# Kernel optimization log

Hardware: AMD Instinct MI355X
Metric: run time of the kernel (lower is better)

Reference implementation:

```python
import jax, jax.numpy as jnp
import numpy as np
import math

IN_CH = 256
CH = 128
SCALE = math.sqrt(CH)
TEMPERATURE = 1.0


def setup_inputs() -> dict:
    key = jax.random.key(0)
    ks = jax.random.split(key, 9)
    B, C, H, W = 8, IN_CH, 56, 56
    x = jax.random.normal(ks[0], (B, C, H, W), dtype=jnp.float32)
    s_in = 1.0 / math.sqrt(IN_CH)
    s_ch = 1.0 / math.sqrt(CH)
    wq = jax.random.uniform(ks[1], (CH, IN_CH), minval=-s_in, maxval=s_in)
    bq = jax.random.uniform(ks[2], (CH,), minval=-s_in, maxval=s_in)
    wk = jax.random.uniform(ks[3], (CH, IN_CH), minval=-s_in, maxval=s_in)
    bk = jax.random.uniform(ks[4], (CH,), minval=-s_in, maxval=s_in)
    wv = jax.random.uniform(ks[5], (CH, IN_CH), minval=-s_in, maxval=s_in)
    bv = jax.random.uniform(ks[6], (CH,), minval=-s_in, maxval=s_in)
    wo = jax.random.uniform(ks[7], (IN_CH, CH), minval=-s_ch, maxval=s_ch)
    bo = jax.random.uniform(ks[8], (IN_CH,), minval=-s_ch, maxval=s_ch)
    return {"x": x, "wq": wq, "bq": bq, "wk": wk, "bk": bk,
            "wv": wv, "bv": bv, "wo": wo, "bo": bo}


def reference(x, wq, bq, wk, bk, wv, bv, wo, bo):
    B, C, H, W = x.shape
    N = H * W
    xf = x.reshape(B, C, N)  # flatten spatial; 1x1 conv == channel matmul
    q = jnp.einsum('oc,bcn->bon', wq, xf) + bq[None, :, None]  # (B,CH,N)
    k = jnp.einsum('oc,bcn->bon', wk, xf) + bk[None, :, None]
    v = jnp.einsum('oc,bcn->bon', wv, xf) + bv[None, :, None]
    # similarity map (B, N, N): query positions x key positions
    sim = jnp.einsum('bcn,bcm->bnm', q, k) / (SCALE * TEMPERATURE)
    attn = jax.nn.softmax(sim, axis=2)
    out = jnp.einsum('bnm,bcm->bnc', attn, v)  # (B, N, CH)
    out = jnp.einsum('oc,bnc->bon', wo, out) + bo[None, :, None]  # (B,IN_CH,N)
    return x + out.reshape(B, C, H, W)
```

## Files before the change

kernel.cpp:

```cpp
#include <hip/hip_runtime.h>
#include <hip/hip_bf16.h>
#include <math.h>

#define NPOS 3136
#define NB   8
#define LOG2E 1.44269504088896f
#define QSCALE (0.08838834764831845f * LOG2E)
#define OFS2  11.54156032711168f

typedef __attribute__((ext_vector_type(8))) short shortx8;
typedef __attribute__((ext_vector_type(4))) short shortx4;
typedef __attribute__((ext_vector_type(4))) float f32x4;
typedef __attribute__((ext_vector_type(16))) float f32x16;
typedef __attribute__((ext_vector_type(4))) unsigned int uint4v;

struct S8pair { shortx4 lo, hi; };

__device__ __forceinline__ unsigned short f2bf(float f) {
    unsigned int i = __builtin_bit_cast(unsigned int, f);
    i += 0x7FFFu + ((i >> 16) & 1u);
    return (unsigned short)(i >> 16);
}
__device__ __forceinline__ void gll16(const unsigned short* g, unsigned short* l) {
    __builtin_amdgcn_global_load_lds((const __attribute__((address_space(1))) void*)g,
                                     (__attribute__((address_space(3))) void*)l, 16, 0, 0);
}

__global__ __launch_bounds__(256) void cast_w(
    const float* __restrict__ wq, const float* __restrict__ wk,
    const float* __restrict__ wv, const float* __restrict__ wo,
    unsigned short* __restrict__ Wb)
{
    const int sel = blockIdx.y;
    const float* src = (sel == 0) ? wq : (sel == 1) ? wk : (sel == 2) ? wv : wo;
    const float sc = (sel == 0) ? QSCALE : 1.0f;
    unsigned short* dst = Wb + sel * 32768;
    int i0 = (blockIdx.x * 256 + threadIdx.x) * 8;
    #pragma unroll
    for (int e = 0; e < 8; ++e) dst[i0 + e] = f2bf(src[i0 + e] * sc);
}

__global__ __launch_bounds__(256) void cast_xT(
    const float* __restrict__ x, unsigned short* __restrict__ xT)
{
    const int b = blockIdx.z, c0 = blockIdx.y * 64, n0 = blockIdx.x * 64;
    __shared__ unsigned short Ls[64 * 66];
    const int t = threadIdx.x;
    {
        int r = t >> 2, q4 = t & 3;
        const float* src = x + ((size_t)b * 256 + c0 + r) * NPOS + n0 + q4 * 16;
        #pragma unroll
        for (int i = 0; i < 16; ++i) Ls[r * 66 + q4 * 16 + i] = f2bf(src[i]);
    }
    __syncthreads();
    {
        int j = t >> 2, h4 = t & 3;
        shortx8 v0, v1;
        #pragma unroll
        for (int i = 0; i < 8; ++i) v0[i] = (short)Ls[(h4 * 16 + i) * 66 + j];
        #pragma unroll
        for (int i = 0; i < 8; ++i) v1[i] = (short)Ls[(h4 * 16 + 8 + i) * 66 + j];
        unsigned short* dst = xT + ((size_t)b * NPOS + n0 + j) * 256 + c0 + h4 * 16;
        *reinterpret_cast<shortx8*>(dst) = v0;
        *reinterpret_cast<shortx8*>(dst + 8) = v1;
    }
}

__global__ __launch_bounds__(256) void qkv_mfma(
    const unsigned short* __restrict__ xT,
    const unsigned short* __restrict__ Wb,
    const float* __restrict__ bq, const float* __restrict__ bk, const float* __restrict__ bv,
    unsigned short* __restrict__ qT, unsigned short* __restrict__ kT,
    unsigned short* __restrict__ vC)
{
    const int b = blockIdx.z, sel = blockIdx.y, n0 = blockIdx.x * 64;
    const int t = threadIdx.x, lane = t & 63, wave = t >> 6;
    const int l16 = lane & 15, lhi = lane >> 4;
    __shared__ __align__(16) unsigned short Wt[128 * 128];
    __shared__ __align__(16) unsigned short Xt[64 * 128];
    const unsigned short* Wsel = Wb + sel * 32768;
    const float* bias = (sel == 0) ? bq : (sel == 1) ? bk : bv;

    f32x4 acc[2][4];
    #pragma unroll
    for (int ab = 0; ab < 2; ++ab)
        #pragma unroll
        for (int nb = 0; nb < 4; ++nb) acc[ab][nb] = f32x4{0.f, 0.f, 0.f, 0.f};

    for (int ks0 = 0; ks0 < 2; ++ks0) {
        const int k0 = ks0 * 128;
        __syncthreads();
        #pragma unroll
        for (int i = 0; i < 8; ++i) {
            int c = (wave * 8 + i) * 64 + lane;
            int row = c >> 4, cin = (c & 15) ^ (row & 7);
            gll16(Wsel + (size_t)row * 256 + k0 + cin * 8, &Wt[0] + (wave * 8 + i) * 512);
        }
        #pragma unroll
        for (int i = 0; i < 4; ++i) {
            int c = (wave * 4 + i) * 64 + lane;
            int row = c >> 4, cin = (c & 15) ^ (row & 7);
            gll16(xT + ((size_t)b * NPOS + n0 + row) * 256 + k0 + cin * 8,
                  &Xt[0] + (wave * 4 + i) * 512);
        }
        __syncthreads();
        #pragma unroll
        for (int ks = 0; ks < 4; ++ks) {
            shortx8 aW[2];
            #pragma unroll
            for (int ab = 0; ab < 2; ++ab) {
                int row = wave * 32 + ab * 16 + l16;
                int idx = (row * 128 + ks * 32 + lhi * 8) ^ ((row & 7) << 3);
                aW[ab] = *reinterpret_cast<const shortx8*>(Wt + idx);
            }
            #pragma unroll
            for (int nb = 0; nb < 4; ++nb) {
                int row = nb * 16 + l16;
                int idx = (row * 128 + ks * 32 + lhi * 8) ^ ((row & 7) << 3);
                shortx8 bX = *reinterpret_cast<const shortx8*>(Xt + idx);
                acc[0][nb] = __builtin_amdgcn_mfma_f32_16x16x32_bf16(aW[0], bX, acc[0][nb], 0, 0, 0);
                acc[1][nb] = __builtin_amdgcn_mfma_f32_16x16x32_bf16(aW[1], bX, acc[1][nb], 0, 0, 0);
            }
        }
    }
    const int strip = wave * 32;
    if (sel < 2) {
        unsigned short* dst0 = ((sel == 0) ? qT : kT) + (size_t)b * NPOS * 128;
        const float bsc = (sel == 0) ? QSCALE : 1.0f;
        #pragma unroll
        for (int ab = 0; ab < 2; ++ab) {
            int ocb = strip + ab * 16 + lhi * 4;
            float bb[4];
            #pragma unroll
            for (int j = 0; j < 4; ++j) bb[j] = bias[ocb + j] * bsc;
            #pragma unroll
            for (int nb = 0; nb < 4; ++nb) {
                int n = n0 + nb * 16 + l16;
                shortx4 u;
                #pragma unroll
                for (int j = 0; j < 4; ++j) u[j] = (short)f2bf(acc[ab][nb][j] + bb[j]);
                *reinterpret_cast<shortx4*>(dst0 + (size_t)n * 128 + ocb) = u;
            }
        }
    } else {
        #pragma unroll
        for (int ab = 0; ab < 2; ++ab)
            #pragma unroll
            for (int j = 0; j < 4; ++j) {
                int oc = strip + ab * 16 + lhi * 4 + j;
                float bb = bias[oc];
                unsigned short* dst = vC + ((size_t)b * 128 + oc) * NPOS + n0;
                #pragma unroll
                for (int nb = 0; nb < 4; ++nb)
                    dst[nb * 16 + l16] = f2bf(acc[ab][nb][j] + bb);
            }
    }
}

__global__ __launch_bounds__(256) void attn_kernel(
    const unsigned short* __restrict__ qT,
    const unsigned short* __restrict__ kT,
    const unsigned short* __restrict__ vC,
    unsigned short* __restrict__ ao,
    float* __restrict__ lrG)
{
    const int b = blockIdx.y, n0 = blockIdx.x * 64;
    const int t = threadIdx.x, lane = t & 63, wave = t >> 6;
    const int l31 = lane & 31, h = lane >> 5;
    const int qsub = wave >> 1, kh = wave & 1;

    __shared__ __align__(16) unsigned short KsB[2][64 * 128];
    __shared__ __align__(16) unsigned short VsB[2][128 * 64];

    shortx8 aQ[8];
    {
        const unsigned short* qp = qT + ((size_t)b * NPOS + n0 + qsub * 32 + l31) * 128 + h * 8;
        #pragma unroll
        for (int kk = 0; kk < 8; ++kk)
            aQ[kk] = *reinterpret_cast<const shortx8*>(qp + kk * 16);
    }

    const unsigned short* kSrc[4];
    const unsigned short* vSrc[4];
    unsigned sDst[4];
    #pragma unroll
    for (int i = 0; i < 4; ++i) {
        int c = (wave * 4 + i) * 64 + lane;
        int rK = c >> 4, cK = (c & 15) ^ (rK & 15);
        kSrc[i] = kT + ((size_t)b * NPOS + rK) * 128 + cK * 8;
        int rV = c >> 3, cV = (c & 7) ^ (rV & 7);
        vSrc[i] = vC + ((size_t)b * 128 + rV) * NPOS + cV * 8;
        sDst[i] = (wave * 4 + i) * 512;
    }

    unsigned kIdx[8];
    {
        int rowK = kh * 32 + l31;
        #pragma unroll
        for (int kk = 0; kk < 8; ++kk)
            kIdx[kk] = rowK * 128 + (((kk * 2 + h) ^ (rowK & 15)) * 8);
    }
    unsigned vIdx[4][2][2];
    #pragma unroll
    for (int ob = 0; ob < 4; ++ob) {
        int rowV = ob * 32 + l31;
        #pragma unroll
        for (int ks = 0; ks < 2; ++ks)
            #pragma unroll
            for (int rr = 0; rr < 2; ++rr)
                vIdx[ob][ks][rr] = rowV * 64 + (((kh * 4 + ks * 2 + rr) ^ (rowV & 7)) * 8) + h * 4;
    }

    f32x16 o[4];
    #pragma unroll
    for (int ob = 0; ob < 4; ++ob)
        #pragma unroll
        for (int r = 0; r < 16; ++r) o[ob][r] = 0.f;
    float lrP = 0.f;

    #pragma unroll
    for (int i = 0; i < 4; ++i) {
        gll16(kSrc[i], &KsB[0][0] + sDst[i]);
        gll16(vSrc[i], &VsB[0][0] + sDst[i]);
    }
    __syncthreads();

    int cur = 0;
    for (int kt = 0; kt < NPOS / 64; ++kt) {
        if (kt + 1 < NPOS / 64) {
            const int m1 = (kt + 1) * 64;
            #pragma unroll
            for (int i = 0; i < 4; ++i) {
                gll16(kSrc[i] + (size_t)m1 * 128, &KsB[cur ^ 1][0] + sDst[i]);
                gll16(vSrc[i] + m1, &VsB[cur ^ 1][0] + sDst[i]);
            }
        }
        const unsigned short* Ks = &KsB[cur][0];
        const unsigned short* Vs = &VsB[cur][0];

        f32x16 sA, sB;
        #pragma unroll
        for (int r = 0; r < 16; ++r) { sA[r] = 0.f; sB[r] = 0.f; }
        #pragma unroll
        for (int kk = 0; kk < 8; kk += 2) {
            shortx8 k0 = *reinterpret_cast<const shortx8*>(Ks + kIdx[kk]);
            shortx8 k1 = *reinterpret_cast<const shortx8*>(Ks + kIdx[kk + 1]);
            sA = __builtin_amdgcn_mfma_f32_32x32x16_bf16(k0, aQ[kk], sA, 0, 0, 0);
            sB = __builtin_amdgcn_mfma_f32_32x32x16_bf16(k1, aQ[kk + 1], sB, 0, 0, 0);
        }

        unsigned pk[8];
        #pragma unroll
        for (int g = 0; g < 4; ++g) {
            float p0 = exp2f(sA[g * 4 + 0] + sB[g * 4 + 0] - OFS2);
            float p1 = exp2f(sA[g * 4 + 1] + sB[g * 4 + 1] - OFS2);
            float p2 = exp2f(sA[g * 4 + 2] + sB[g * 4 + 2] - OFS2);
            float p3 = exp2f(sA[g * 4 + 3] + sB[g * 4 + 3] - OFS2);
            lrP += (p0 + p1) + (p2 + p3);
            asm("v_cvt_pk_bf16_f32 %0, %1, %2" : "=v"(pk[g * 2 + 0]) : "v"(p0), "v"(p1));
            asm("v_cvt_pk_bf16_f32 %0, %1, %2" : "=v"(pk[g * 2 + 1]) : "v"(p2), "v"(p3));
        }

        #pragma unroll
        for (int ks = 0; ks < 2; ++ks) {
            uint4v pv = {pk[ks * 4 + 0], pk[ks * 4 + 1], pk[ks * 4 + 2], pk[ks * 4 + 3]};
            shortx8 PA = __builtin_bit_cast(shortx8, pv);
            #pragma unroll
            for (int ob = 0; ob < 4; ++ob) {
                shortx4 lo = *reinterpret_cast<const shortx4*>(Vs + vIdx[ob][ks][0]);
                shortx4 hi = *reinterpret_cast<const shortx4*>(Vs + vIdx[ob][ks][1]);
                shortx8 bV = __builtin_bit_cast(shortx8, S8pair{lo, hi});
                o[ob] = __builtin_amdgcn_mfma_f32_32x32x16_bf16(PA, bV, o[ob], 0, 0, 0);
            }
        }
        __syncthreads();
        cur ^= 1;
    }

    float lr2 = lrP + __shfl_xor(lrP, 32);
    float* Om = reinterpret_cast<float*>(&KsB[0][0]);
    float* lrS = reinterpret_cast<float*>(&VsB[1][0]);
    unsigned short* Oo = &VsB[0][0];

    if (kh == 1) {
        #pragma unroll
        for (int ob = 0; ob < 4; ++ob)
            #pragma unroll
            for (int r = 0; r < 16; ++r) {
                int q = qsub * 32 + (r & 3) + 8 * (r >> 2) + 4 * h;
                Om[q * 128 + ob * 32 + l31] = o[ob][r];
            }
        if (lane < 32) lrS[qsub * 32 + l31] = lr2;
    }
    __syncthreads();
    if (kh == 0) {
        #pragma unroll
        for (int ob = 0; ob < 4; ++ob)
            #pragma unroll
            for (int r = 0; r < 16; ++r) {
                int q = qsub * 32 + (r & 3) + 8 * (r >> 2) + 4 * h;
                int idx = q * 128 + ob * 32 + l31;
                Oo[idx] = f2bf(o[ob][r] + Om[idx]);
            }
        if (lane < 32)
            lrG[(size_t)b * NPOS + n0 + qsub * 32 + l31] = lr2 + lrS[qsub * 32 + l31];
    }
    __syncthreads();
    {
        const shortx8* src = reinterpret_cast<const shortx8*>(Oo);
        shortx8* dst = reinterpret_cast<shortx8*>(ao + ((size_t)b * NPOS + n0) * 128);
        #pragma unroll
        for (int i = 0; i < 4; ++i) dst[t + 256 * i] = src[t + 256 * i];
    }
}

__global__ __launch_bounds__(256) void out_proj(
    const float* __restrict__ x,
    const unsigned short* __restrict__ Wb,
    const float* __restrict__ bo,
    const unsigned short* __restrict__ ao,
    const float* __restrict__ lrG,
    float* __restrict__ y)
{
    const int b = blockIdx.y, n0 = blockIdx.x * 64;
    const int t = threadIdx.x, lane = t & 63, wave = t >> 6;
    const int l16 = lane & 15, lhi = lane >> 4;
    __shared__ __align__(16) unsigned short Wt[256 * 128];
    __shared__ __align__(16) unsigned short At[64 * 128];
    const unsigned short* wo = Wb + 98304;

    #pragma unroll
    for (int i = 0; i < 16; ++i) {
        int c = (wave * 16 + i) * 64 + lane;
        int row = c >> 4, cin = (c & 15) ^ (row & 7);
        gll16(wo + (size_t)row * 128 + cin * 8, &Wt[0] + (wave * 16 + i) * 512);
    }
    #pragma unroll
    for (int i = 0; i < 4; ++i) {
        int c = (wave * 4 + i) * 64 + lane;
        int row = c >> 4, cin = (c & 15) ^ (row & 7);
        gll16(ao + ((size_t)b * NPOS + n0 + row) * 128 + cin * 8, &At[0] + (wave * 4 + i) * 512);
    }
    __syncthreads();

    f32x4 acc[4][4];
    #pragma unroll
    for (int ab = 0; ab < 4; ++ab)
        #pragma unroll
        for (int nb = 0; nb < 4; ++nb) acc[ab][nb] = f32x4{0.f, 0.f, 0.f, 0.f};

    const int strip = wave * 64;
    #pragma unroll
    for (int ks = 0; ks < 4; ++ks) {
        shortx8 aW[4];
        #pragma unroll
        for (int ab = 0; ab < 4; ++ab) {
            int row = strip + ab * 16 + l16;
            int idx = (row * 128 + ks * 32 + lhi * 8) ^ ((row & 7) << 3);
            aW[ab] = *reinterpret_cast<const shortx8*>(Wt + idx);
        }
        #pragma unroll
        for (int nb = 0; nb < 4; ++nb) {
            int row = nb * 16 + l16;
            int idx = (row * 128 + ks * 32 + lhi * 8) ^ ((row & 7) << 3);
            shortx8 bA = *reinterpret_cast<const shortx8*>(At + idx);
            #pragma unroll
            for (int ab = 0; ab < 4; ++ab)
                acc[ab][nb] = __builtin_amdgcn_mfma_f32_16x16x32_bf16(aW[ab], bA, acc[ab][nb], 0, 0, 0);
        }
    }

    float inv[4];
    #pragma unroll
    for (int nb = 0; nb < 4; ++nb)
        inv[nb] = 1.0f / lrG[(size_t)b * NPOS + n0 + nb * 16 + l16];

    #pragma unroll
    for (int ab = 0; ab < 4; ++ab)
        #pragma unroll
        for (int j = 0; j < 4; ++j) {
            int oc = strip + ab * 16 + lhi * 4 + j;
            float bb = bo[oc];
            const float* xr = x + ((size_t)b * 256 + oc) * NPOS + n0;
            float* yr = y + ((size_t)b * 256 + oc) * NPOS + n0;
            #pragma unroll
            for (int nb = 0; nb < 4; ++nb) {
                int n = nb * 16 + l16;
                yr[n] = xr[n] + bb + acc[ab][nb][j] * inv[nb];
            }
        }
}

extern "C" void kernel_launch(void* const* d_in, const int* in_sizes, int n_in,
                              void* d_out, int out_size, void* d_ws, size_t ws_size,
                              hipStream_t stream)
{
    const float* x  = (const float*)d_in[0];
    const float* wq = (const float*)d_in[1];
    const float* bq = (const float*)d_in[2];
    const float* wk = (const float*)d_in[3];
    const float* bk = (const float*)d_in[4];
    const float* wv = (const float*)d_in[5];
    const float* bv = (const float*)d_in[6];
    const float* wo = (const float*)d_in[7];
    const float* bo = (const float*)d_in[8];
    float* y = (float*)d_out;

    const size_t sz = (size_t)NB * NPOS * 128;
    unsigned short* qT = (unsigned short*)d_ws;
    unsigned short* kT = qT + sz;
    unsigned short* vC = kT + sz;
    unsigned short* xT = vC + sz;
    unsigned short* ao = xT;
    unsigned short* Wb = xT + 2 * sz;
    float* lrG = (float*)(Wb + 131072);

    cast_w  <<<dim3(16, 4),       256, 0, stream>>>(wq, wk, wv, wo, Wb);
    cast_xT <<<dim3(49, 4, NB),   256, 0, stream>>>(x, xT);
    qkv_mfma<<<dim3(49, 3, NB),   256, 0, stream>>>(xT, Wb, bq, bk, bv, qT, kT, vC);
    attn_kernel<<<dim3(49, NB),   256, 0, stream>>>(qT, kT, vC, ao, lrG);
    out_proj<<<dim3(49, NB),      256, 0, stream>>>(x, Wb, bo, ao, lrG, y);
}
```

Measured before the change: 130.1 us.

## Split attention key range across two blocks and merge partial outputs

Launches the attention kernel with a second grid dimension that splits the 49 key tiles into two halves, doubling the block count from 392 to 784 so more of the GPU's compute units get work. Each half writes its own bf16 partial output and row-sum, and a new merge kernel adds the two outputs before out_proj sums the row-sums. To fit more blocks per CU, LDS is cut to a single buffer (no double-buffered prefetch) and launch bounds request 4 blocks per CU. In exchange it loses load/compute overlap, adds an extra kernel pass over the output, and adds bf16 rounding of the partial sums.

```diff
diff --git a/kernel.cpp b/kernel.cpp
--- a/kernel.cpp
+++ b/kernel.cpp
@@ -16,6 +16,10 @@
 
 struct S8pair { shortx4 lo, hi; };
 
+__device__ __forceinline__ float bf2f(unsigned short u) {
+    unsigned int i = ((unsigned int)u) << 16;
+    return __builtin_bit_cast(float, i);
+}
 __device__ __forceinline__ unsigned short f2bf(float f) {
     unsigned int i = __builtin_bit_cast(unsigned int, f);
     i += 0x7FFFu + ((i >> 16) & 1u);
@@ -157,20 +161,23 @@
     }
 }
 
-__global__ __launch_bounds__(256) void attn_kernel(
+__global__ __launch_bounds__(256, 4) void attn_kernel(
     const unsigned short* __restrict__ qT,
     const unsigned short* __restrict__ kT,
     const unsigned short* __restrict__ vC,
     unsigned short* __restrict__ ao,
     float* __restrict__ lrG)
 {
-    const int b = blockIdx.y, n0 = blockIdx.x * 64;
+    const int b = blockIdx.y, n0 = blockIdx.x * 64, z = blockIdx.z;
+    const int kt0 = z ? 25 : 0, kt1 = z ? 49 : 25;
     const int t = threadIdx.x, lane = t & 63, wave = t >> 6;
     const int l31 = lane & 31, h = lane >> 5;
     const int qsub = wave >> 1, kh = wave & 1;
 
-    __shared__ __align__(16) unsigned short KsB[2][64 * 128];
-    __shared__ __align__(16) unsigned short VsB[2][128 * 64];
+    __shared__ __align__(16) unsigned short SM[64 * 128 * 2 + 128];
+    unsigned short* Ks = SM;
+    unsigned short* Vs = SM + 8192;
+    float* lrS = reinterpret_cast<float*>(SM + 16384);
 
     shortx8 aQ[8];
     {
@@ -180,16 +187,14 @@
             aQ[kk] = *reinterpret_cast<const shortx8*>(qp + kk * 16);
     }
 
-    const unsigned short* kSrc[4];
-    const unsigned short* vSrc[4];
-    unsigned sDst[4];
+    unsigned kOff[4], vOff[4], sDst[4];
     #pragma unroll
     for (int i = 0; i < 4; ++i) {
         int c = (wave * 4 + i) * 64 + lane;
         int rK = c >> 4, cK = (c & 15) ^ (rK & 15);
-        kSrc[i] = kT + ((size_t)b * NPOS + rK) * 128 + cK * 8;
+        kOff[i] = ((unsigned)b * NPOS + rK) * 128 + cK * 8;
         int rV = c >> 3, cV = (c & 7) ^ (rV & 7);
-        vSrc[i] = vC + ((size_t)b * 128 + rV) * NPOS + cV * 8;
+        vOff[i] = ((unsigned)b * 128 + rV) * NPOS + cV * 8;
         sDst[i] = (wave * 4 + i) * 512;
     }
 
@@ -200,15 +205,12 @@
         for (int kk = 0; kk < 8; ++kk)
             kIdx[kk] = rowK * 128 + (((kk * 2 + h) ^ (rowK & 15)) * 8);
     }
-    unsigned vIdx[4][2][2];
+    unsigned vBase[4], vM8[4];
     #pragma unroll
     for (int ob = 0; ob < 4; ++ob) {
         int rowV = ob * 32 + l31;
-        #pragma unroll
-        for (int ks = 0; ks < 2; ++ks)
-            #pragma unroll
-            for (int rr = 0; rr < 2; ++rr)
-                vIdx[ob][ks][rr] = rowV * 64 + (((kh * 4 + ks * 2 + rr) ^ (rowV & 7)) * 8) + h * 4;
+        vBase[ob] = rowV * 64 + h * 4;
+        vM8[ob] = (rowV & 7) * 8;
     }
 
     f32x16 o[4];
@@ -218,25 +220,18 @@
         for (int r = 0; r < 16; ++r) o[ob][r] = 0.f;
     float lrP = 0.f;
 
-    #pragma unroll
-    for (int i = 0; i < 4; ++i) {
-        gll16(kSrc[i], &KsB[0][0] + sDst[i]);
-        gll16(vSrc[i], &VsB[0][0] + sDst[i]);
-    }
-    __syncthreads();
-
-    int cur = 0;
-    for (int kt = 0; kt < NPOS / 64; ++kt) {
-        if (kt + 1 < NPOS / 64) {
-            const int m1 = (kt + 1) * 64;
+    for (int kt = kt0; kt < kt1; ++kt) {
+        if (kt > kt0) __syncthreads();
+        {
+            const unsigned short* kP = kT + (size_t)kt * 8192;
+            const unsigned short* vP = vC + kt * 64;
             #pragma unroll
             for (int i = 0; i < 4; ++i) {
-                gll16(kSrc[i] + (size_t)m1 * 128, &KsB[cur ^ 1][0] + sDst[i]);
-                gll16(vSrc[i] + m1, &VsB[cur ^ 1][0] + sDst[i]);
-            }
-        }
-        const unsigned short* Ks = &KsB[cur][0];
-        const unsigned short* Vs = &VsB[cur][0];
+                gll16(kP + kOff[i], Ks + sDst[i]);
+                gll16(vP + vOff[i], Vs + sDst[i]);
+            }
+        }
+        __syncthreads();
 
         f32x16 sA, sB;
         #pragma unroll
@@ -267,28 +262,26 @@
             shortx8 PA = __builtin_bit_cast(shortx8, pv);
             #pragma unroll
             for (int ob = 0; ob < 4; ++ob) {
-                shortx4 lo = *reinterpret_cast<const shortx4*>(Vs + vIdx[ob][ks][0]);
-                shortx4 hi = *reinterpret_cast<const shortx4*>(Vs + vIdx[ob][ks][1]);
+                unsigned i0 = vBase[ob] + (((kh * 4 + ks * 2 + 0) * 8) ^ vM8[ob]);
+                unsigned i1 = vBase[ob] + (((kh * 4 + ks * 2 + 1) * 8) ^ vM8[ob]);
+                shortx4 lo = *reinterpret_cast<const shortx4*>(Vs + i0);
+                shortx4 hi = *reinterpret_cast<const shortx4*>(Vs + i1);
                 shortx8 bV = __builtin_bit_cast(shortx8, S8pair{lo, hi});
                 o[ob] = __builtin_amdgcn_mfma_f32_32x32x16_bf16(PA, bV, o[ob], 0, 0, 0);
             }
         }
-        __syncthreads();
-        cur ^= 1;
-    }
-
+    }
+    __syncthreads();
+
+    unsigned short* OmB = Ks;
     float lr2 = lrP + __shfl_xor(lrP, 32);
-    float* Om = reinterpret_cast<float*>(&KsB[0][0]);
-    float* lrS = reinterpret_cast<float*>(&VsB[1][0]);
-    unsigned short* Oo = &VsB[0][0];
-
     if (kh == 1) {
         #pragma unroll
         for (int ob = 0; ob < 4; ++ob)
             #pragma unroll
             for (int r = 0; r < 16; ++r) {
                 int q = qsub * 32 + (r & 3) + 8 * (r >> 2) + 4 * h;
-                Om[q * 128 + ob * 32 + l31] = o[ob][r];
+                OmB[q * 128 + ob * 32 + l31] = f2bf(o[ob][r]);
             }
         if (lane < 32) lrS[qsub * 32 + l31] = lr2;
     }
@@ -300,18 +293,33 @@
             for (int r = 0; r < 16; ++r) {
                 int q = qsub * 32 + (r & 3) + 8 * (r >> 2) + 4 * h;
                 int idx = q * 128 + ob * 32 + l31;
-                Oo[idx] = f2bf(o[ob][r] + Om[idx]);
+                OmB[idx] = f2bf(o[ob][r] + bf2f(OmB[idx]));
             }
         if (lane < 32)
-            lrG[(size_t)b * NPOS + n0 + qsub * 32 + l31] = lr2 + lrS[qsub * 32 + l31];
+            lrG[((size_t)z * NB + b) * NPOS + n0 + qsub * 32 + l31]
+                = lr2 + lrS[qsub * 32 + l31];
     }
     __syncthreads();
     {
-        const shortx8* src = reinterpret_cast<const shortx8*>(Oo);
-        shortx8* dst = reinterpret_cast<shortx8*>(ao + ((size_t)b * NPOS + n0) * 128);
+        const shortx8* src = reinterpret_cast<const shortx8*>(OmB);
+        shortx8* dst = reinterpret_cast<shortx8*>(
+            ao + (((size_t)z * NB + b) * NPOS + n0) * 128);
         #pragma unroll
         for (int i = 0; i < 4; ++i) dst[t + 256 * i] = src[t + 256 * i];
     }
+}
+
+__global__ __launch_bounds__(256) void merge_ao(
+    unsigned short* __restrict__ a1, const unsigned short* __restrict__ a2)
+{
+    size_t i = ((size_t)blockIdx.x * 256 + threadIdx.x) * 8;
+    shortx8 u = *reinterpret_cast<const shortx8*>(a1 + i);
+    shortx8 v = *reinterpret_cast<const shortx8*>(a2 + i);
+    shortx8 w;
+    #pragma unroll
+    for (int e = 0; e < 8; ++e)
+        w[e] = (short)f2bf(bf2f((unsigned short)u[e]) + bf2f((unsigned short)v[e]));
+    *reinterpret_cast<shortx8*>(a1 + i) = w;
 }
 
 __global__ __launch_bounds__(256) void out_proj(
@@ -372,8 +380,10 @@
 
     float inv[4];
     #pragma unroll
-    for (int nb = 0; nb < 4; ++nb)
-        inv[nb] = 1.0f / lrG[(size_t)b * NPOS + n0 + nb * 16 + l16];
+    for (int nb = 0; nb < 4; ++nb) {
+        size_t n = (size_t)b * NPOS + n0 + nb * 16 + l16;
+        inv[nb] = 1.0f / (lrG[n] + lrG[(size_t)NB * NPOS + n]);
+    }
 
     #pragma unroll
     for (int ab = 0; ab < 4; ++ab)
@@ -418,6 +428,7 @@
     cast_w  <<<dim3(16, 4),       256, 0, stream>>>(wq, wk, wv, wo, Wb);
     cast_xT <<<dim3(49, 4, NB),   256, 0, stream>>>(x, xT);
     qkv_mfma<<<dim3(49, 3, NB),   256, 0, stream>>>(xT, Wb, bq, bk, bv, qT, kT, vC);
-    attn_kernel<<<dim3(49, NB),   256, 0, stream>>>(qT, kT, vC, ao, lrG);
+    attn_kernel<<<dim3(49, NB, 2), 256, 0, stream>>>(qT, kT, vC, ao, lrG);
+    merge_ao<<<dim3(1568),        256, 0, stream>>>(ao, ao + sz);
     out_proj<<<dim3(49, NB),      256, 0, stream>>>(x, Wb, bo, ao, lrG, y);
 }
```

Measured after the change: 257.9 us. 98.2% more time.

## Single-buffer V tile in attention loop to fit three blocks per CU

Applied to the files above, without the earlier changes.

The attention kernel drops V double-buffering to shrink LDS use and raises launch bounds to three blocks per CU. The next K tile is still prefetched, while the current V tile is loaded at the start of each iteration and waited on with an explicit vmcnt before the PV MFMAs. s_setprio is raised around both MFMA phases. The aims are higher occupancy and hiding the V load behind the QK phase; the cost is a tighter register budget and no workgroup barrier between the vmcnt wait and reading V tiles written by other waves, which risks a race.

```diff
diff --git a/kernel.cpp b/kernel.cpp
--- a/kernel.cpp
+++ b/kernel.cpp
@@ -16,6 +16,10 @@
 
 struct S8pair { shortx4 lo, hi; };
 
+__device__ __forceinline__ float bf2f(unsigned short u) {
+    unsigned int i = ((unsigned int)u) << 16;
+    return __builtin_bit_cast(float, i);
+}
 __device__ __forceinline__ unsigned short f2bf(float f) {
     unsigned int i = __builtin_bit_cast(unsigned int, f);
     i += 0x7FFFu + ((i >> 16) & 1u);
@@ -157,7 +161,7 @@
     }
 }
 
-__global__ __launch_bounds__(256) void attn_kernel(
+__global__ __launch_bounds__(256, 3) void attn_kernel(
     const unsigned short* __restrict__ qT,
     const unsigned short* __restrict__ kT,
     const unsigned short* __restrict__ vC,
@@ -170,7 +174,8 @@
     const int qsub = wave >> 1, kh = wave & 1;
 
     __shared__ __align__(16) unsigned short KsB[2][64 * 128];
-    __shared__ __align__(16) unsigned short VsB[2][128 * 64];
+    __shared__ __align__(16) unsigned short Vs[128 * 64];
+    __shared__ float lrS[64];
 
     shortx8 aQ[8];
     {
@@ -180,16 +185,14 @@
             aQ[kk] = *reinterpret_cast<const shortx8*>(qp + kk * 16);
     }
 
-    const unsigned short* kSrc[4];
-    const unsigned short* vSrc[4];
-    unsigned sDst[4];
+    unsigned kOff[4], vOff[4], sDst[4];
     #pragma unroll
     for (int i = 0; i < 4; ++i) {
         int c = (wave * 4 + i) * 64 + lane;
         int rK = c >> 4, cK = (c & 15) ^ (rK & 15);
-        kSrc[i] = kT + ((size_t)b * NPOS + rK) * 128 + cK * 8;
+        kOff[i] = rK * 128 + cK * 8;
         int rV = c >> 3, cV = (c & 7) ^ (rV & 7);
-        vSrc[i] = vC + ((size_t)b * 128 + rV) * NPOS + cV * 8;
+        vOff[i] = rV * NPOS + cV * 8;
         sDst[i] = (wave * 4 + i) * 512;
     }
 
@@ -200,15 +203,12 @@
         for (int kk = 0; kk < 8; ++kk)
             kIdx[kk] = rowK * 128 + (((kk * 2 + h) ^ (rowK & 15)) * 8);
     }
-    unsigned vIdx[4][2][2];
+    unsigned vBase[4], vM8[4];
     #pragma unroll
     for (int ob = 0; ob < 4; ++ob) {
         int rowV = ob * 32 + l31;
-        #pragma unroll
-        for (int ks = 0; ks < 2; ++ks)
-            #pragma unroll
-            for (int rr = 0; rr < 2; ++rr)
-                vIdx[ob][ks][rr] = rowV * 64 + (((kh * 4 + ks * 2 + rr) ^ (rowV & 7)) * 8) + h * 4;
+        vBase[ob] = rowV * 64 + h * 4;
+        vM8[ob] = (rowV & 7) * 8;
     }
 
     f32x16 o[4];
@@ -218,69 +218,92 @@
         for (int r = 0; r < 16; ++r) o[ob][r] = 0.f;
     float lrP = 0.f;
 
-    #pragma unroll
-    for (int i = 0; i < 4; ++i) {
-        gll16(kSrc[i], &KsB[0][0] + sDst[i]);
-        gll16(vSrc[i], &VsB[0][0] + sDst[i]);
-    }
+    const unsigned short* kTb = kT + (size_t)b * NPOS * 128;
+    const unsigned short* vCb = vC + (size_t)b * 128 * NPOS;
+
+    #pragma unroll
+    for (int i = 0; i < 4; ++i) gll16(vCb + vOff[i], Vs + sDst[i]);
+    #pragma unroll
+    for (int i = 0; i < 4; ++i) gll16(kTb + kOff[i], &KsB[0][0] + sDst[i]);
     __syncthreads();
 
     int cur = 0;
-    for (int kt = 0; kt < NPOS / 64; ++kt) {
-        if (kt + 1 < NPOS / 64) {
-            const int m1 = (kt + 1) * 64;
-            #pragma unroll
-            for (int i = 0; i < 4; ++i) {
-                gll16(kSrc[i] + (size_t)m1 * 128, &KsB[cur ^ 1][0] + sDst[i]);
-                gll16(vSrc[i] + m1, &VsB[cur ^ 1][0] + sDst[i]);
-            }
-        }
+    #define QK_PHASE(KSP)                                                            \
+        f32x16 sA, sB;                                                               \
+        _Pragma("unroll")                                                            \
+        for (int r = 0; r < 16; ++r) { sA[r] = 0.f; sB[r] = 0.f; }                   \
+        __builtin_amdgcn_s_setprio(1);                                               \
+        _Pragma("unroll")                                                            \
+        for (int kk = 0; kk < 8; kk += 2) {                                          \
+            shortx8 k0 = *reinterpret_cast<const shortx8*>(KSP + kIdx[kk]);          \
+            shortx8 k1 = *reinterpret_cast<const shortx8*>(KSP + kIdx[kk + 1]);      \
+            sA = __builtin_amdgcn_mfma_f32_32x32x16_bf16(k0, aQ[kk], sA, 0, 0, 0);   \
+            sB = __builtin_amdgcn_mfma_f32_32x32x16_bf16(k1, aQ[kk + 1], sB, 0, 0, 0);\
+        }                                                                            \
+        __builtin_amdgcn_s_setprio(0);                                               \
+        unsigned pk[8];                                                              \
+        _Pragma("unroll")                                                            \
+        for (int g = 0; g < 4; ++g) {                                                \
+            float p0 = exp2f(sA[g * 4 + 0] + sB[g * 4 + 0] - OFS2);                  \
+            float p1 = exp2f(sA[g * 4 + 1] + sB[g * 4 + 1] - OFS2);                  \
+            float p2 = exp2f(sA[g * 4 + 2] + sB[g * 4 + 2] - OFS2);                  \
+            float p3 = exp2f(sA[g * 4 + 3] + sB[g * 4 + 3] - OFS2);                  \
+            lrP += (p0 + p1) + (p2 + p3);                                            \
+            asm("v_cvt_pk_bf16_f32 %0, %1, %2" : "=v"(pk[g * 2 + 0]) : "v"(p0), "v"(p1)); \
+            asm("v_cvt_pk_bf16_f32 %0, %1, %2" : "=v"(pk[g * 2 + 1]) : "v"(p2), "v"(p3)); \
+        }
+
+    #define PV_PHASE                                                                 \
+        __builtin_amdgcn_s_setprio(1);                                               \
+        _Pragma("unroll")                                                            \
+        for (int ks = 0; ks < 2; ++ks) {                                             \
+            uint4v pv = {pk[ks * 4 + 0], pk[ks * 4 + 1], pk[ks * 4 + 2], pk[ks * 4 + 3]}; \
+            shortx8 PA = __builtin_bit_cast(shortx8, pv);                            \
+            _Pragma("unroll")                                                        \
+            for (int ob = 0; ob < 4; ++ob) {                                         \
+                unsigned i0 = vBase[ob] + (((kh * 4 + ks * 2 + 0) * 8) ^ vM8[ob]);   \
+                unsigned i1 = vBase[ob] + (((kh * 4 + ks * 2 + 1) * 8) ^ vM8[ob]);   \
+                shortx4 lo = *reinterpret_cast<const shortx4*>(Vs + i0);             \
+                shortx4 hi = *reinterpret_cast<const shortx4*>(Vs + i1);             \
+                shortx8 bV = __builtin_bit_cast(shortx8, S8pair{lo, hi});            \
+                o[ob] = __builtin_amdgcn_mfma_f32_32x32x16_bf16(PA, bV, o[ob], 0, 0, 0); \
+            }                                                                        \
+        }                                                                            \
+        __builtin_amdgcn_s_setprio(0);
+
+    for (int kt = 0; kt < NPOS / 64 - 1; ++kt) {
+        if (kt > 0) {
+            #pragma unroll
+            for (int i = 0; i < 4; ++i)
+                gll16(vCb + kt * 64 + vOff[i], Vs + sDst[i]);
+        }
+        #pragma unroll
+        for (int i = 0; i < 4; ++i)
+            gll16(kTb + (kt + 1) * 8192 + kOff[i], &KsB[cur ^ 1][0] + sDst[i]);
+
         const unsigned short* Ks = &KsB[cur][0];
-        const unsigned short* Vs = &VsB[cur][0];
-
-        f32x16 sA, sB;
-        #pragma unroll
-        for (int r = 0; r < 16; ++r) { sA[r] = 0.f; sB[r] = 0.f; }
-        #pragma unroll
-        for (int kk = 0; kk < 8; kk += 2) {
-            shortx8 k0 = *reinterpret_cast<const shortx8*>(Ks + kIdx[kk]);
-            shortx8 k1 = *reinterpret_cast<const shortx8*>(Ks + kIdx[kk + 1]);
-            sA = __builtin_amdgcn_mfma_f32_32x32x16_bf16(k0, aQ[kk], sA, 0, 0, 0);
-            sB = __builtin_amdgcn_mfma_f32_32x32x16_bf16(k1, aQ[kk + 1], sB, 0, 0, 0);
-        }
-
-        unsigned pk[8];
-        #pragma unroll
-        for (int g = 0; g < 4; ++g) {
-            float p0 = exp2f(sA[g * 4 + 0] + sB[g * 4 + 0] - OFS2);
-            float p1 = exp2f(sA[g * 4 + 1] + sB[g * 4 + 1] - OFS2);
-            float p2 = exp2f(sA[g * 4 + 2] + sB[g * 4 + 2] - OFS2);
-            float p3 = exp2f(sA[g * 4 + 3] + sB[g * 4 + 3] - OFS2);
-            lrP += (p0 + p1) + (p2 + p3);
-            asm("v_cvt_pk_bf16_f32 %0, %1, %2" : "=v"(pk[g * 2 + 0]) : "v"(p0), "v"(p1));
-            asm("v_cvt_pk_bf16_f32 %0, %1, %2" : "=v"(pk[g * 2 + 1]) : "v"(p2), "v"(p3));
-        }
-
-        #pragma unroll
-        for (int ks = 0; ks < 2; ++ks) {
-            uint4v pv = {pk[ks * 4 + 0], pk[ks * 4 + 1], pk[ks * 4 + 2], pk[ks * 4 + 3]};
-            shortx8 PA = __builtin_bit_cast(shortx8, pv);
-            #pragma unroll
-            for (int ob = 0; ob < 4; ++ob) {
-                shortx4 lo = *reinterpret_cast<const shortx4*>(Vs + vIdx[ob][ks][0]);
-                shortx4 hi = *reinterpret_cast<const shortx4*>(Vs + vIdx[ob][ks][1]);
-                shortx8 bV = __builtin_bit_cast(shortx8, S8pair{lo, hi});
-                o[ob] = __builtin_amdgcn_mfma_f32_32x32x16_bf16(PA, bV, o[ob], 0, 0, 0);
-            }
-        }
+        QK_PHASE(Ks)
+        asm volatile("s_waitcnt vmcnt(4)" ::: "memory");
+        __builtin_amdgcn_sched_barrier(0);
+        PV_PHASE
         __syncthreads();
         cur ^= 1;
     }
+    {
+        #pragma unroll
+        for (int i = 0; i < 4; ++i)
+            gll16(vCb + (NPOS / 64 - 1) * 64 + vOff[i], Vs + sDst[i]);
+        const unsigned short* Ks = &KsB[cur][0];
+        QK_PHASE(Ks)
+        asm volatile("s_waitcnt vmcnt(0)" ::: "memory");
+        __builtin_amdgcn_sched_barrier(0);
+        PV_PHASE
+    }
+    __syncthreads();
 
     float lr2 = lrP + __shfl_xor(lrP, 32);
     float* Om = reinterpret_cast<float*>(&KsB[0][0]);
-    float* lrS = reinterpret_cast<float*>(&VsB[1][0]);
-    unsigned short* Oo = &VsB[0][0];
+    unsigned short* Oo = &Vs[0];
 
     if (kh == 1) {
         #pragma unroll
@@ -312,6 +335,8 @@
         #pragma unroll
         for (int i = 0; i < 4; ++i) dst[t + 256 * i] = src[t + 256 * i];
     }
+    #undef QK_PHASE
+    #undef PV_PHASE
 }
 
 __global__ __launch_bounds__(256) void out_proj(
```

Result: slower. 168.6 us (+29.6%).

## Deepen attention K/V prefetch pipeline with explicit vmcnt waits and wave priority

Applied to the files above, without the earlier changes.

Restructures the attention main loop to keep two tiles of K/V in flight. Explicit s_waitcnt vmcnt(8) and raw s_barrier calls replace the full __syncthreads drain, so loads for tile kt+1 stay outstanding while tile kt is computed. It also raises wave priority around the MFMA sections, remaps block indices so consecutive blocks cover different batches, and computes the V swizzle indices inline to free registers. The risks are a stricter LDS buffer-reuse ordering that depends on correct waitcnt accounting, and possible scheduling changes from the sched_barriers.

```diff
diff --git a/kernel.cpp b/kernel.cpp
--- a/kernel.cpp
+++ b/kernel.cpp
@@ -16,6 +16,10 @@
 
 struct S8pair { shortx4 lo, hi; };
 
+__device__ __forceinline__ float bf2f(unsigned short u) {
+    unsigned int i = ((unsigned int)u) << 16;
+    return __builtin_bit_cast(float, i);
+}
 __device__ __forceinline__ unsigned short f2bf(float f) {
     unsigned int i = __builtin_bit_cast(unsigned int, f);
     i += 0x7FFFu + ((i >> 16) & 1u);
@@ -164,10 +168,13 @@
     unsigned short* __restrict__ ao,
     float* __restrict__ lrG)
 {
-    const int b = blockIdx.y, n0 = blockIdx.x * 64;
+    const int i_lin = blockIdx.y * 49 + blockIdx.x;
+    const int b = i_lin & 7;
+    const int n0 = (i_lin >> 3) * 64;
     const int t = threadIdx.x, lane = t & 63, wave = t >> 6;
     const int l31 = lane & 31, h = lane >> 5;
     const int qsub = wave >> 1, kh = wave & 1;
+    const int NT = NPOS / 64;
 
     __shared__ __align__(16) unsigned short KsB[2][64 * 128];
     __shared__ __align__(16) unsigned short VsB[2][128 * 64];
@@ -200,15 +207,12 @@
         for (int kk = 0; kk < 8; ++kk)
             kIdx[kk] = rowK * 128 + (((kk * 2 + h) ^ (rowK & 15)) * 8);
     }
-    unsigned vIdx[4][2][2];
+    unsigned vBase[4], vM8[4];
     #pragma unroll
     for (int ob = 0; ob < 4; ++ob) {
         int rowV = ob * 32 + l31;
-        #pragma unroll
-        for (int ks = 0; ks < 2; ++ks)
-            #pragma unroll
-            for (int rr = 0; rr < 2; ++rr)
-                vIdx[ob][ks][rr] = rowV * 64 + (((kh * 4 + ks * 2 + rr) ^ (rowV & 7)) * 8) + h * 4;
+        vBase[ob] = rowV * 64 + h * 4;
+        vM8[ob] = (rowV & 7) * 8;
     }
 
     f32x16 o[4];
@@ -218,64 +222,79 @@
         for (int r = 0; r < 16; ++r) o[ob][r] = 0.f;
     float lrP = 0.f;
 
-    #pragma unroll
-    for (int i = 0; i < 4; ++i) {
-        gll16(kSrc[i], &KsB[0][0] + sDst[i]);
-        gll16(vSrc[i], &VsB[0][0] + sDst[i]);
+    #define STAGE(kt_, buf_)                                                          \
+        _Pragma("unroll")                                                             \
+        for (int i = 0; i < 4; ++i) {                                                 \
+            gll16(kSrc[i] + (size_t)(kt_) * 8192, &KsB[buf_][0] + sDst[i]);           \
+            gll16(vSrc[i] + (kt_) * 64, &VsB[buf_][0] + sDst[i]);                     \
+        }
+
+    #define COMPUTE(Ks, Vs)                                                           \
+    {                                                                                 \
+        f32x16 sA, sB;                                                                \
+        _Pragma("unroll")                                                             \
+        for (int r = 0; r < 16; ++r) { sA[r] = 0.f; sB[r] = 0.f; }                    \
+        __builtin_amdgcn_s_setprio(1);                                                \
+        _Pragma("unroll")                                                             \
+        for (int kk = 0; kk < 8; kk += 2) {                                           \
+            shortx8 k0 = *reinterpret_cast<const shortx8*>((Ks) + kIdx[kk]);          \
+            shortx8 k1 = *reinterpret_cast<const shortx8*>((Ks) + kIdx[kk + 1]);      \
+            sA = __builtin_amdgcn_mfma_f32_32x32x16_bf16(k0, aQ[kk], sA, 0, 0, 0);    \
+            sB = __builtin_amdgcn_mfma_f32_32x32x16_bf16(k1, aQ[kk + 1], sB, 0, 0, 0);\
+        }                                                                             \
+        __builtin_amdgcn_s_setprio(0);                                                \
+        unsigned pk[8];                                                               \
+        _Pragma("unroll")                                                             \
+        for (int g = 0; g < 4; ++g) {                                                 \
+            float p0 = exp2f(sA[g * 4 + 0] + sB[g * 4 + 0] - OFS2);                   \
+            float p1 = exp2f(sA[g * 4 + 1] + sB[g * 4 + 1] - OFS2);                   \
+            float p2 = exp2f(sA[g * 4 + 2] + sB[g * 4 + 2] - OFS2);                   \
+            float p3 = exp2f(sA[g * 4 + 3] + sB[g * 4 + 3] - OFS2);                   \
+            lrP += (p0 + p1) + (p2 + p3);                                             \
+            asm("v_cvt_pk_bf16_f32 %0, %1, %2" : "=v"(pk[g * 2 + 0]) : "v"(p0), "v"(p1)); \
+            asm("v_cvt_pk_bf16_f32 %0, %1, %2" : "=v"(pk[g * 2 + 1]) : "v"(p2), "v"(p3)); \
+        }                                                                             \
+        __builtin_amdgcn_s_setprio(1);                                                \
+        _Pragma("unroll")                                                             \
+        for (int ks = 0; ks < 2; ++ks) {                                              \
+            uint4v pv = {pk[ks * 4 + 0], pk[ks * 4 + 1], pk[ks * 4 + 2], pk[ks * 4 + 3]}; \
+            shortx8 PA = __builtin_bit_cast(shortx8, pv);                             \
+            _Pragma("unroll")                                                         \
+            for (int ob = 0; ob < 4; ++ob) {                                          \
+                unsigned i0 = vBase[ob] + (((kh * 4 + ks * 2 + 0) * 8) ^ vM8[ob]);    \
+                unsigned i1 = vBase[ob] + (((kh * 4 + ks * 2 + 1) * 8) ^ vM8[ob]);    \
+                shortx4 lo = *reinterpret_cast<const shortx4*>((Vs) + i0);            \
+                shortx4 hi = *reinterpret_cast<const shortx4*>((Vs) + i1);            \
+                shortx8 bV = __builtin_bit_cast(shortx8, S8pair{lo, hi});             \
+                o[ob] = __builtin_amdgcn_mfma_f32_32x32x16_bf16(PA, bV, o[ob], 0, 0, 0); \
+            }                                                                         \
+        }                                                                             \
+        __builtin_amdgcn_s_setprio(0);                                                \
+    }
+
+    STAGE(0, 0)
+    STAGE(1, 1)
+
+    int cur = 0;
+    for (int kt = 0; kt < NT - 1; ++kt) {
+        asm volatile("s_waitcnt vmcnt(8)" ::: "memory");
+        __builtin_amdgcn_sched_barrier(0);
+        __builtin_amdgcn_s_barrier();
+        __builtin_amdgcn_sched_barrier(0);
+        COMPUTE(&KsB[cur][0], &VsB[cur][0])
+        __builtin_amdgcn_sched_barrier(0);
+        __builtin_amdgcn_s_barrier();
+        __builtin_amdgcn_sched_barrier(0);
+        if (kt < NT - 2) { STAGE(kt + 2, cur) }
+        cur ^= 1;
+    }
+    {
+        asm volatile("s_waitcnt vmcnt(0)" ::: "memory");
+        __builtin_amdgcn_sched_barrier(0);
+        __builtin_amdgcn_s_barrier();
+        COMPUTE(&KsB[cur][0], &VsB[cur][0])
     }
     __syncthreads();
-
-    int cur = 0;
-    for (int kt = 0; kt < NPOS / 64; ++kt) {
-        if (kt + 1 < NPOS / 64) {
-            const int m1 = (kt + 1) * 64;
-            #pragma unroll
-            for (int i = 0; i < 4; ++i) {
-                gll16(kSrc[i] + (size_t)m1 * 128, &KsB[cur ^ 1][0] + sDst[i]);
-                gll16(vSrc[i] + m1, &VsB[cur ^ 1][0] + sDst[i]);
-            }
-        }
-        const unsigned short* Ks = &KsB[cur][0];
-        const unsigned short* Vs = &VsB[cur][0];
-
-        f32x16 sA, sB;
-        #pragma unroll
-        for (int r = 0; r < 16; ++r) { sA[r] = 0.f; sB[r] = 0.f; }
-        #pragma unroll
-        for (int kk = 0; kk < 8; kk += 2) {
-            shortx8 k0 = *reinterpret_cast<const shortx8*>(Ks + kIdx[kk]);
-            shortx8 k1 = *reinterpret_cast<const shortx8*>(Ks + kIdx[kk + 1]);
-            sA = __builtin_amdgcn_mfma_f32_32x32x16_bf16(k0, aQ[kk], sA, 0, 0, 0);
-            sB = __builtin_amdgcn_mfma_f32_32x32x16_bf16(k1, aQ[kk + 1], sB, 0, 0, 0);
-        }
-
-        unsigned pk[8];
-        #pragma unroll
-        for (int g = 0; g < 4; ++g) {
-            float p0 = exp2f(sA[g * 4 + 0] + sB[g * 4 + 0] - OFS2);
-            float p1 = exp2f(sA[g * 4 + 1] + sB[g * 4 + 1] - OFS2);
-            float p2 = exp2f(sA[g * 4 + 2] + sB[g * 4 + 2] - OFS2);
-            float p3 = exp2f(sA[g * 4 + 3] + sB[g * 4 + 3] - OFS2);
-            lrP += (p0 + p1) + (p2 + p3);
-            asm("v_cvt_pk_bf16_f32 %0, %1, %2" : "=v"(pk[g * 2 + 0]) : "v"(p0), "v"(p1));
-            asm("v_cvt_pk_bf16_f32 %0, %1, %2" : "=v"(pk[g * 2 + 1]) : "v"(p2), "v"(p3));
-        }
-
-        #pragma unroll
-        for (int ks = 0; ks < 2; ++ks) {
-            uint4v pv = {pk[ks * 4 + 0], pk[ks * 4 + 1], pk[ks * 4 + 2], pk[ks * 4 + 3]};
-            shortx8 PA = __builtin_bit_cast(shortx8, pv);
-            #pragma unroll
-            for (int ob = 0; ob < 4; ++ob) {
-                shortx4 lo = *reinterpret_cast<const shortx4*>(Vs + vIdx[ob][ks][0]);
-                shortx4 hi = *reinterpret_cast<const shortx4*>(Vs + vIdx[ob][ks][1]);
-                shortx8 bV = __builtin_bit_cast(shortx8, S8pair{lo, hi});
-                o[ob] = __builtin_amdgcn_mfma_f32_32x32x16_bf16(PA, bV, o[ob], 0, 0, 0);
-            }
-        }
-        __syncthreads();
-        cur ^= 1;
-    }
 
     float lr2 = lrP + __shfl_xor(lrP, 32);
     float* Om = reinterpret_cast<float*>(&KsB[0][0]);
@@ -312,6 +331,8 @@
         #pragma unroll
         for (int i = 0; i < 4; ++i) dst[t + 256 * i] = src[t + 256 * i];
     }
+    #undef STAGE
+    #undef COMPUTE
 }
 
 __global__ __launch_bounds__(256) void out_proj(
```

After: 122.2 us. 6.1% less time.
